# Optimization experiments

Measured on AMD Instinct MI355X. Metric: run time of the kernel, lower is better.

## Reference

```python
import jax, jax.numpy as jnp
import numpy as np

NUM_BUOYS = 16384
TIME_STEPS = 8
FEATURE_DIM = 64
ID_EMB_DIM = 1024  # must equal gru_hidden_size for steps 4/5 to type-check
HIDDEN = 1024
NUM_EMB = 100
INPUT_SIZE = FEATURE_DIM + ID_EMB_DIM


def setup_inputs() -> dict:
    key = jax.random.key(0)
    k = jax.random.split(key, 7)
    s = 1.0 / np.sqrt(HIDDEN)
    return {
        "buoy_obs": jax.random.normal(k[0], (NUM_BUOYS, TIME_STEPS, FEATURE_DIM), jnp.float32),
        "buoy_ids": jax.random.randint(k[1], (NUM_BUOYS,), 0, NUM_EMB),
        "emb": jax.random.normal(k[2], (NUM_EMB, ID_EMB_DIM), jnp.float32),
        "W_ih": jax.random.uniform(k[3], (3 * HIDDEN, INPUT_SIZE), jnp.float32, -s, s),
        "W_hh": jax.random.uniform(k[4], (3 * HIDDEN, HIDDEN), jnp.float32, -s, s),
        "b_ih": jax.random.uniform(k[5], (3 * HIDDEN,), jnp.float32, -s, s),
        "b_hh": jax.random.uniform(k[6], (3 * HIDDEN,), jnp.float32, -s, s),
    }


def _gru_cell(x, h, W_ih, W_hh, b_ih, b_hh):
    # PyTorch GRU gate layout: [r, z, n]
    gi = x @ W_ih.T + b_ih  # (N, 3H)
    gh = h @ W_hh.T + b_hh  # (N, 3H)
    gi_r, gi_z, gi_n = jnp.split(gi, 3, axis=-1)
    gh_r, gh_z, gh_n = jnp.split(gh, 3, axis=-1)
    r = jax.nn.sigmoid(gi_r + gh_r)
    z = jax.nn.sigmoid(gi_z + gh_z)
    n = jnp.tanh(gi_n + r * gh_n)
    return (1.0 - z) * n + z * h


def reference(buoy_obs, buoy_ids, emb, W_ih, W_hh, b_ih, b_hh):
    num_buoys = buoy_obs.shape[0]
    id_emb = emb[buoy_ids]  # (N, E)
    h = jnp.zeros((num_buoys, HIDDEN), buoy_obs.dtype)
    outs = []
    # three unrolled steps: input = [obs_t, id_emb]
    for t in range(3):
        x = jnp.concatenate([buoy_obs[:, t, :], id_emb], axis=-1)
        h = _gru_cell(x, h, W_ih, W_hh, b_ih, b_hh)
        outs.append(h)
    # step 4: input = [out0, obs_1]
    x = jnp.concatenate([outs[0], buoy_obs[:, 1, :]], axis=-1)
    h = _gru_cell(x, h, W_ih, W_hh, b_ih, b_hh)
    second_out = h
    # step 5: input = [out4, obs_2]
    x = jnp.concatenate([second_out, buoy_obs[:, 2, :]], axis=-1)
    h = _gru_cell(x, h, W_ih, W_hh, b_ih, b_hh)
    # AdaptiveMaxPool1d(1) over a length-1 time axis is identity
    return h[None, :, :]  # (1, N, H)
```

## Files before the change

kernel.cpp:

```cpp
#include <hip/hip_runtime.h>
#include <hip/hip_bf16.h>


typedef __bf16 bf16_4 __attribute__((ext_vector_type(4)));
typedef __bf16 bf16_8 __attribute__((ext_vector_type(8)));
typedef float  f32_16 __attribute__((ext_vector_type(16)));

#define NBUOY 16384
#define HID   1024

__device__ __forceinline__ void async16(const void* g, void* l) {
    __builtin_amdgcn_global_load_lds(
        (const __attribute__((address_space(1))) unsigned int*)g,
        (__attribute__((address_space(3))) unsigned int*)l, 16, 0, 0);
}
__device__ __forceinline__ float sigm(float x)  { return 1.f / (1.f + __expf(-x)); }
__device__ __forceinline__ float tanh_f(float x){ return 1.f - 2.f / (1.f + __expf(2.f * x)); }

template<int QN, int K>
__device__ __forceinline__ void phase_loop(
    const __bf16* __restrict__ Ap, long sA, int aRow0,
    const __bf16* __restrict__ Wp, long sW, int n0,
    __bf16* lsA, __bf16* lsB, f32_16 acc[4][2], int tid)
{
    const int lane = tid & 63, wid = tid >> 6;
    const int wm = wid >> 1, wn = wid & 1;
    const int l31 = lane & 31, hi = lane >> 5, l7 = lane & 7;
    const int srow = tid >> 3, schunk = tid & 7;

    auto stage = [&](int buf, int k0) {
        __bf16* la = lsA + buf * (128 * 64);
        __bf16* lb = lsB + buf * (192 * 64);
        #pragma unroll
        for (int r = 0; r < 4; ++r) {
            int row = r * 32 + srow;
            int lc  = schunk ^ (row & 7);
            async16(Ap + (long)(aRow0 + row) * sA + k0 + lc * 8,
                    la + (r * 32 + wid * 8) * 64);
        }
        #pragma unroll
        for (int r = 0; r < 6; ++r) {
            int brow = r * 32 + srow;
            int lc   = schunk ^ (brow & 7);
            async16(Wp + (long)((brow >> 6) * 1024 + n0 + (brow & 63)) * sW + k0 + lc * 8,
                    lb + (r * 32 + wid * 8) * 64);
        }
    };

    __syncthreads();
    stage(0, 0);
    int cur = 0;

    #pragma unroll 1
    for (int k0 = 0; k0 < K; k0 += 64) {
        __syncthreads();
        if (k0 + 64 < K) stage(cur ^ 1, k0 + 64);

        const __bf16* la = lsA + cur * (128 * 64);
        const __bf16* lb = lsB + cur * (192 * 64);
        #pragma unroll
        for (int ks = 0; ks < 4; ++ks) {
            int pc = (((ks * 2 + hi) ^ l7)) * 8;
            bf16_8 a0 = *(const bf16_8*)(la + (wm * 64 +      l31) * 64 + pc);
            bf16_8 a1 = *(const bf16_8*)(la + (wm * 64 + 32 + l31) * 64 + pc);
            bf16_8 br = *(const bf16_8*)(lb + (        wn * 32 + l31) * 64 + pc);
            bf16_8 bz = *(const bf16_8*)(lb + ( 64 +   wn * 32 + l31) * 64 + pc);
            bf16_8 bn = *(const bf16_8*)(lb + (128 +   wn * 32 + l31) * 64 + pc);
            acc[0][0]  = __builtin_amdgcn_mfma_f32_32x32x16_bf16(a0, br, acc[0][0], 0, 0, 0);
            acc[0][1]  = __builtin_amdgcn_mfma_f32_32x32x16_bf16(a1, br, acc[0][1], 0, 0, 0);
            acc[1][0]  = __builtin_amdgcn_mfma_f32_32x32x16_bf16(a0, bz, acc[1][0], 0, 0, 0);
            acc[1][1]  = __builtin_amdgcn_mfma_f32_32x32x16_bf16(a1, bz, acc[1][1], 0, 0, 0);
            acc[QN][0] = __builtin_amdgcn_mfma_f32_32x32x16_bf16(a0, bn, acc[QN][0], 0, 0, 0);
            acc[QN][1] = __builtin_amdgcn_mfma_f32_32x32x16_bf16(a1, bn, acc[QN][1], 0, 0, 0);
        }
        cur ^= 1;
    }
}

template<int KIH, int KHH, bool USE_E, bool OUT_F32>
__global__ __launch_bounds__(256, 2)
void gru_step(const __bf16* __restrict__ Aih, long sAih,
              const __bf16* __restrict__ Wih,
              const __bf16* __restrict__ Ahh,
              const __bf16* __restrict__ Whh,
              const float*  __restrict__ E,
              const int*    __restrict__ ids,
              const float*  __restrict__ bih,
              const float*  __restrict__ bhh,
              const __bf16* __restrict__ hprev,
              void* __restrict__ outp, long sOut)
{
    __shared__ __bf16 lsA[2 * 128 * 64];
    __shared__ __bf16 lsB[2 * 192 * 64];
    const int tid  = threadIdx.x;
    const int lane = tid & 63, wid = tid >> 6;
    const int wm = wid >> 1, wn = wid & 1;
    const int l31 = lane & 31, hi = lane >> 5;
    const int m0 = blockIdx.y * 128;
    const int n0 = blockIdx.x * 64;

    f32_16 acc[4][2];
    #pragma unroll
    for (int q = 0; q < 4; ++q)
        #pragma unroll
        for (int mt = 0; mt < 2; ++mt) acc[q][mt] = (f32_16)(0.0f);

    phase_loop<2, KIH>(Aih, sAih, m0, Wih, 1088, n0, lsA, lsB, acc, tid);
    if (KHH > 0)
        phase_loop<3, KHH>(Ahh, 1088, m0, Whh, 1024, n0, lsA, lsB, acc, tid);

    const int col = n0 + wn * 32 + l31;
    const float bhr = bhh[col], bhz = bhh[1024 + col], bhn = bhh[2048 + col];
    float cir = 0.f, ciz = 0.f, cin = 0.f;
    if (!USE_E) { cir = bih[col]; ciz = bih[1024 + col]; cin = bih[2048 + col]; }

    #pragma unroll
    for (int mt = 0; mt < 2; ++mt) {
        const int rowb = m0 + wm * 64 + mt * 32 + 4 * hi;
        #pragma unroll
        for (int reg = 0; reg < 16; ++reg) {
            const int row = rowb + (reg & 3) + 8 * (reg >> 2);
            float er = cir, ez = ciz, en = cin;
            if (USE_E) {
                const float* Ep = E + (long)ids[row] * 3072 + col;
                er = Ep[0]; ez = Ep[1024]; en = Ep[2048];
            }
            const float r  = sigm(acc[0][mt][reg] + er + bhr);
            const float z  = sigm(acc[1][mt][reg] + ez + bhz);
            const float nn = tanh_f(acc[2][mt][reg] + en + r * (acc[3][mt][reg] + bhn));
            float hp = 0.f;
            if (KHH > 0) hp = (float)hprev[(long)row * 1088 + col];
            const float h = (1.f - z) * nn + z * hp;
            if (OUT_F32) ((float*)outp)[(long)row * sOut + col] = h;
            else        ((__bf16*)outp)[(long)row * sOut + col] = (__bf16)h;
        }
    }
}

#define ETILE 10
__global__ void compute_E(const float* __restrict__ emb, const float* __restrict__ Wih,
                          const float* __restrict__ bih, float* __restrict__ E)
{
    __shared__ float semb[ETILE * 1024];
    const int e0 = blockIdx.x * ETILE;
    const int j  = blockIdx.y * 256 + threadIdx.x;
    for (int i = threadIdx.x; i < ETILE * 1024; i += 256)
        semb[i] = emb[(long)(e0 + (i >> 10)) * 1024 + (i & 1023)];
    __syncthreads();
    const float* wp = Wih + (long)j * 1088 + 64;
    float a[ETILE];
    const float b = bih[j];
    #pragma unroll
    for (int t = 0; t < ETILE; ++t) a[t] = b;
    for (int k = 0; k < 1024; k += 4) {
        const float4 w = *(const float4*)(wp + k);
        #pragma unroll
        for (int t = 0; t < ETILE; ++t) {
            const float* se = semb + t * 1024 + k;
            a[t] += se[0] * w.x + se[1] * w.y + se[2] * w.z + se[3] * w.w;
        }
    }
    #pragma unroll
    for (int t = 0; t < ETILE; ++t) E[(long)(e0 + t) * 3072 + j] = a[t];
}

__global__ void build_obs(const float* __restrict__ obs, __bf16* __restrict__ OBS,
                          __bf16* __restrict__ X0, __bf16* __restrict__ X1)
{
    const int q = blockIdx.x * 256 + threadIdx.x;
    const int row = q / 48, w = (q % 48) * 4;
    const float4 v = *(const float4*)(obs + (long)row * 512 + w);
    bf16_4 b; b[0] = (__bf16)v.x; b[1] = (__bf16)v.y; b[2] = (__bf16)v.z; b[3] = (__bf16)v.w;
    *(bf16_4*)(OBS + (long)row * 192 + w) = b;
    if (w >= 64 && w < 128) *(bf16_4*)(X0 + (long)row * 1088 + 1024 + (w - 64))  = b;
    if (w >= 128)           *(bf16_4*)(X1 + (long)row * 1088 + 1024 + (w - 128)) = b;
}

__global__ void cast_f32_bf16(const float* __restrict__ s, __bf16* __restrict__ d, int n4)
{
    const int i = blockIdx.x * 256 + threadIdx.x;
    if (i < n4) {
        const float4 v = ((const float4*)s)[i];
        bf16_4 b; b[0] = (__bf16)v.x; b[1] = (__bf16)v.y; b[2] = (__bf16)v.z; b[3] = (__bf16)v.w;
        ((bf16_4*)d)[i] = b;
    }
}

extern "C" void kernel_launch(void* const* d_in, const int* in_sizes, int n_in,
                              void* d_out, int out_size, void* d_ws, size_t ws_size,
                              hipStream_t stream)
{
    const float* obs = (const float*)d_in[0];
    const int*   ids = (const int*)  d_in[1];
    const float* emb = (const float*)d_in[2];
    const float* Wih = (const float*)d_in[3];
    const float* Whh = (const float*)d_in[4];
    const float* bih = (const float*)d_in[5];
    const float* bhh = (const float*)d_in[6];
    float* out = (float*)d_out;

    const size_t MB = 1 << 20;
    const size_t XB = (size_t)NBUOY * 1088 * 2;
    const size_t NEEDED = 21 * MB + 3 * XB;
    if (ws_size < NEEDED) return;

    char* ws = (char*)d_ws;
    float*  E   = (float*) ws;
    __bf16* Wb  = (__bf16*)(ws + 2 * MB);
    __bf16* Ub  = (__bf16*)(ws + 9 * MB);
    __bf16* OBS = (__bf16*)(ws + 15 * MB);
    __bf16* X0  = (__bf16*)(ws + 21 * MB);
    __bf16* X1  = (__bf16*)(ws + 21 * MB + XB);
    __bf16* X2  = (__bf16*)(ws + 21 * MB + 2 * XB);

    dim3 blk(256);
    dim3 gridG(HID / 64, NBUOY / 128);

    cast_f32_bf16<<<(3072 * 1088 / 4 + 255) / 256, blk, 0, stream>>>(Wih, Wb, 3072 * 1088 / 4);
    cast_f32_bf16<<<(3072 * 1024 / 4 + 255) / 256, blk, 0, stream>>>(Whh, Ub, 3072 * 1024 / 4);
    build_obs<<<NBUOY * 48 / 256, blk, 0, stream>>>(obs, OBS, X0, X1);
    compute_E<<<dim3(10, 12), blk, 0, stream>>>(emb, Wih, bih, E);

    gru_step<64, 0, true, false><<<gridG, blk, 0, stream>>>(
        OBS + 0, 192, Wb, nullptr, Ub, E, ids, bih, bhh, nullptr, X0, 1088);
    gru_step<64, 1024, true, false><<<gridG, blk, 0, stream>>>(
        OBS + 64, 192, Wb, X0, Ub, E, ids, bih, bhh, X0, X1, 1088);
    gru_step<64, 1024, true, false><<<gridG, blk, 0, stream>>>(
        OBS + 128, 192, Wb, X1, Ub, E, ids, bih, bhh, X1, X2, 1088);
    gru_step<1088, 1024, false, false><<<gridG, blk, 0, stream>>>(
        X0, 1088, Wb, X2, Ub, nullptr, ids, bih, bhh, X2, X1, 1088);
    gru_step<1088, 1024, false, true><<<gridG, blk, 0, stream>>>(
        X1, 1088, Wb, X1, Ub, nullptr, ids, bih, bhh, X1, out, 1024);
}
```

Before: 1.003 ms.

## Load GEMM operands directly from global into registers, dropping LDS staging

```diff
diff --git a/kernel.cpp b/kernel.cpp
--- a/kernel.cpp
+++ b/kernel.cpp
@@ -9,72 +9,63 @@
 #define NBUOY 16384
 #define HID   1024
 
-__device__ __forceinline__ void async16(const void* g, void* l) {
-    __builtin_amdgcn_global_load_lds(
-        (const __attribute__((address_space(1))) unsigned int*)g,
-        (__attribute__((address_space(3))) unsigned int*)l, 16, 0, 0);
-}
 __device__ __forceinline__ float sigm(float x)  { return 1.f / (1.f + __expf(-x)); }
 __device__ __forceinline__ float tanh_f(float x){ return 1.f - 2.f / (1.f + __expf(2.f * x)); }
 
+#define LOADH(a0, a1, br, bz, bn)                                   \
+    a0[0] = *(const bf16_8*)(pa0);      a0[1] = *(const bf16_8*)(pa0 + 16); \
+    a1[0] = *(const bf16_8*)(pa1);      a1[1] = *(const bf16_8*)(pa1 + 16); \
+    br[0] = *(const bf16_8*)(pbr);      br[1] = *(const bf16_8*)(pbr + 16); \
+    bz[0] = *(const bf16_8*)(pbz);      bz[1] = *(const bf16_8*)(pbz + 16); \
+    bn[0] = *(const bf16_8*)(pbn);      bn[1] = *(const bf16_8*)(pbn + 16); \
+    pa0 += 32; pa1 += 32; pbr += 32; pbz += 32; pbn += 32;
+
+#define MFMAH(a0, a1, br, bz, bn)                                                         \
+    acc[0][0]  = __builtin_amdgcn_mfma_f32_32x32x16_bf16(a0[0], br[0], acc[0][0], 0,0,0); \
+    acc[0][1]  = __builtin_amdgcn_mfma_f32_32x32x16_bf16(a1[0], br[0], acc[0][1], 0,0,0); \
+    acc[1][0]  = __builtin_amdgcn_mfma_f32_32x32x16_bf16(a0[0], bz[0], acc[1][0], 0,0,0); \
+    acc[1][1]  = __builtin_amdgcn_mfma_f32_32x32x16_bf16(a1[0], bz[0], acc[1][1], 0,0,0); \
+    acc[QN][0] = __builtin_amdgcn_mfma_f32_32x32x16_bf16(a0[0], bn[0], acc[QN][0],0,0,0); \
+    acc[QN][1] = __builtin_amdgcn_mfma_f32_32x32x16_bf16(a1[0], bn[0], acc[QN][1],0,0,0); \
+    acc[0][0]  = __builtin_amdgcn_mfma_f32_32x32x16_bf16(a0[1], br[1], acc[0][0], 0,0,0); \
+    acc[0][1]  = __builtin_amdgcn_mfma_f32_32x32x16_bf16(a1[1], br[1], acc[0][1], 0,0,0); \
+    acc[1][0]  = __builtin_amdgcn_mfma_f32_32x32x16_bf16(a0[1], bz[1], acc[1][0], 0,0,0); \
+    acc[1][1]  = __builtin_amdgcn_mfma_f32_32x32x16_bf16(a1[1], bz[1], acc[1][1], 0,0,0); \
+    acc[QN][0] = __builtin_amdgcn_mfma_f32_32x32x16_bf16(a0[1], bn[1], acc[QN][0],0,0,0); \
+    acc[QN][1] = __builtin_amdgcn_mfma_f32_32x32x16_bf16(a1[1], bn[1], acc[QN][1],0,0,0);
+
 template<int QN, int K>
-__device__ __forceinline__ void phase_loop(
+__device__ __forceinline__ void phase_direct(
     const __bf16* __restrict__ Ap, long sA, int aRow0,
     const __bf16* __restrict__ Wp, long sW, int n0,
-    __bf16* lsA, __bf16* lsB, f32_16 acc[4][2], int tid)
+    f32_16 acc[4][2], int tid)
 {
     const int lane = tid & 63, wid = tid >> 6;
     const int wm = wid >> 1, wn = wid & 1;
-    const int l31 = lane & 31, hi = lane >> 5, l7 = lane & 7;
-    const int srow = tid >> 3, schunk = tid & 7;
-
-    auto stage = [&](int buf, int k0) {
-        __bf16* la = lsA + buf * (128 * 64);
-        __bf16* lb = lsB + buf * (192 * 64);
-        #pragma unroll
-        for (int r = 0; r < 4; ++r) {
-            int row = r * 32 + srow;
-            int lc  = schunk ^ (row & 7);
-            async16(Ap + (long)(aRow0 + row) * sA + k0 + lc * 8,
-                    la + (r * 32 + wid * 8) * 64);
-        }
-        #pragma unroll
-        for (int r = 0; r < 6; ++r) {
-            int brow = r * 32 + srow;
-            int lc   = schunk ^ (brow & 7);
-            async16(Wp + (long)((brow >> 6) * 1024 + n0 + (brow & 63)) * sW + k0 + lc * 8,
-                    lb + (r * 32 + wid * 8) * 64);
-        }
-    };
-
-    __syncthreads();
-    stage(0, 0);
-    int cur = 0;
+    const int l31 = lane & 31, hi = lane >> 5;
+
+    const __bf16* pa0 = Ap + (long)(aRow0 + wm * 64 +      l31) * sA + hi * 8;
+    const __bf16* pa1 = Ap + (long)(aRow0 + wm * 64 + 32 + l31) * sA + hi * 8;
+    const __bf16* pbr = Wp + (long)(       n0 + wn * 32 + l31) * sW + hi * 8;
+    const __bf16* pbz = Wp + (long)(1024 + n0 + wn * 32 + l31) * sW + hi * 8;
+    const __bf16* pbn = Wp + (long)(2048 + n0 + wn * 32 + l31) * sW + hi * 8;
+
+    bf16_8 Xa0[2], Xa1[2], Xbr[2], Xbz[2], Xbn[2];
+    bf16_8 Ya0[2], Ya1[2], Ybr[2], Ybz[2], Ybn[2];
+
+    constexpr int S = K / 32;
+    LOADH(Xa0, Xa1, Xbr, Xbz, Xbn)
 
     #pragma unroll 1
-    for (int k0 = 0; k0 < K; k0 += 64) {
-        __syncthreads();
-        if (k0 + 64 < K) stage(cur ^ 1, k0 + 64);
-
-        const __bf16* la = lsA + cur * (128 * 64);
-        const __bf16* lb = lsB + cur * (192 * 64);
-        #pragma unroll
-        for (int ks = 0; ks < 4; ++ks) {
-            int pc = (((ks * 2 + hi) ^ l7)) * 8;
-            bf16_8 a0 = *(const bf16_8*)(la + (wm * 64 +      l31) * 64 + pc);
-            bf16_8 a1 = *(const bf16_8*)(la + (wm * 64 + 32 + l31) * 64 + pc);
-            bf16_8 br = *(const bf16_8*)(lb + (        wn * 32 + l31) * 64 + pc);
-            bf16_8 bz = *(const bf16_8*)(lb + ( 64 +   wn * 32 + l31) * 64 + pc);
-            bf16_8 bn = *(const bf16_8*)(lb + (128 +   wn * 32 + l31) * 64 + pc);
-            acc[0][0]  = __builtin_amdgcn_mfma_f32_32x32x16_bf16(a0, br, acc[0][0], 0, 0, 0);
-            acc[0][1]  = __builtin_amdgcn_mfma_f32_32x32x16_bf16(a1, br, acc[0][1], 0, 0, 0);
-            acc[1][0]  = __builtin_amdgcn_mfma_f32_32x32x16_bf16(a0, bz, acc[1][0], 0, 0, 0);
-            acc[1][1]  = __builtin_amdgcn_mfma_f32_32x32x16_bf16(a1, bz, acc[1][1], 0, 0, 0);
-            acc[QN][0] = __builtin_amdgcn_mfma_f32_32x32x16_bf16(a0, bn, acc[QN][0], 0, 0, 0);
-            acc[QN][1] = __builtin_amdgcn_mfma_f32_32x32x16_bf16(a1, bn, acc[QN][1], 0, 0, 0);
-        }
-        cur ^= 1;
-    }
+    for (int s = 0; s + 2 < S; s += 2) {
+        LOADH(Ya0, Ya1, Ybr, Ybz, Ybn)
+        MFMAH(Xa0, Xa1, Xbr, Xbz, Xbn)
+        LOADH(Xa0, Xa1, Xbr, Xbz, Xbn)
+        MFMAH(Ya0, Ya1, Ybr, Ybz, Ybn)
+    }
+    LOADH(Ya0, Ya1, Ybr, Ybz, Ybn)
+    MFMAH(Xa0, Xa1, Xbr, Xbz, Xbn)
+    MFMAH(Ya0, Ya1, Ybr, Ybz, Ybn)
 }
 
 template<int KIH, int KHH, bool USE_E, bool OUT_F32>
@@ -90,8 +81,6 @@
               const __bf16* __restrict__ hprev,
               void* __restrict__ outp, long sOut)
 {
-    __shared__ __bf16 lsA[2 * 128 * 64];
-    __shared__ __bf16 lsB[2 * 192 * 64];
     const int tid  = threadIdx.x;
     const int lane = tid & 63, wid = tid >> 6;
     const int wm = wid >> 1, wn = wid & 1;
@@ -105,9 +94,9 @@
         #pragma unroll
         for (int mt = 0; mt < 2; ++mt) acc[q][mt] = (f32_16)(0.0f);
 
-    phase_loop<2, KIH>(Aih, sAih, m0, Wih, 1088, n0, lsA, lsB, acc, tid);
+    phase_direct<2, KIH>(Aih, sAih, m0, Wih, 1088, n0, acc, tid);
     if (KHH > 0)
-        phase_loop<3, KHH>(Ahh, 1088, m0, Whh, 1024, n0, lsA, lsB, acc, tid);
+        phase_direct<3, KHH>(Ahh, 1088, m0, Whh, 1024, n0, acc, tid);
 
     const int col = n0 + wn * 32 + l31;
     const float bhr = bhh[col], bhz = bhh[1024 + col], bhn = bhh[2048 + col];
```

Result: slower. 2.101 ms (+109.4%).
